# Kernel tuning notes

Hardware: AMD Instinct MI355X
Metric: run time of the kernel (lower is better)

Reference implementation:

```python
import jax, jax.numpy as jnp
import numpy as np
import math

B, S, IN_DIM = 4, 2048, 512
D, H, L, FF = 256, 4, 4, 2048
HD = D // H
EPS = 1e-5


def _pos_encoding(S, D, dtype=jnp.float32):
    pos = jnp.arange(S, dtype=jnp.float32)[:, None]
    div = jnp.exp(jnp.arange(0, D, 2, dtype=jnp.float32) * (-math.log(10000.0) / D))
    pe = jnp.zeros((S, D), dtype=jnp.float32)
    pe = pe.at[:, 0::2].set(jnp.sin(pos * div))
    pe = pe.at[:, 1::2].set(jnp.cos(pos * div))
    return pe.astype(dtype)


def _layernorm(x, w, b):
    mu = jnp.mean(x, axis=-1, keepdims=True)
    var = jnp.var(x, axis=-1, keepdims=True)
    return (x - mu) * jax.lax.rsqrt(var + EPS) * w + b


def setup_inputs() -> dict:
    key = jax.random.key(0)
    ks = jax.random.split(key, 12)
    sc = 0.02
    inp = {
        "x": jax.random.normal(ks[0], (B, S, IN_DIM), dtype=jnp.float32),
        "W_in": jax.random.normal(ks[1], (D, IN_DIM), dtype=jnp.float32) * sc,
        "b_in": jnp.zeros((D,), dtype=jnp.float32),
        "qkv_w": jax.random.normal(ks[2], (L, 3 * D, D), dtype=jnp.float32) * sc,
        "qkv_b": jnp.zeros((L, 3 * D), dtype=jnp.float32),
        "out_w": jax.random.normal(ks[3], (L, D, D), dtype=jnp.float32) * sc,
        "out_b": jnp.zeros((L, D), dtype=jnp.float32),
        "ln1_w": jnp.ones((L, D), dtype=jnp.float32),
        "ln1_b": jnp.zeros((L, D), dtype=jnp.float32),
        "ff1_w": jax.random.normal(ks[4], (L, FF, D), dtype=jnp.float32) * sc,
        "ff1_b": jnp.zeros((L, FF), dtype=jnp.float32),
        "ff2_w": jax.random.normal(ks[5], (L, D, FF), dtype=jnp.float32) * sc,
        "ff2_b": jnp.zeros((L, D), dtype=jnp.float32),
        "ln2_w": jnp.ones((L, D), dtype=jnp.float32),
        "ln2_b": jnp.zeros((L, D), dtype=jnp.float32),
        "W_fc": jax.random.normal(ks[6], (IN_DIM, D), dtype=jnp.float32) * sc,
        "b_fc": jnp.zeros((IN_DIM,), dtype=jnp.float32),
    }
    return inp


def reference(x, W_in, b_in, qkv_w, qkv_b, out_w, out_b, ln1_w, ln1_b,
              ff1_w, ff1_b, ff2_w, ff2_b, ln2_w, ln2_b, W_fc, b_fc):
    # input projection + positional encoding (dropout=0 / eval)
    h = jnp.einsum('bsi,di->bsd', x, W_in) + b_in
    h = h + _pos_encoding(S, D, h.dtype)[None]

    scale = 1.0 / math.sqrt(HD)
    for l in range(L):
        # --- self-attention (unfused: explicit QK^T + softmax + V) ---
        qkv = jnp.einsum('bsd,ed->bse', h, qkv_w[l]) + qkv_b[l]  # [B,S,3D]
        q, k, v = jnp.split(qkv, 3, axis=-1)
        q = q.reshape(B, S, H, HD).transpose(0, 2, 1, 3)  # [B,H,S,HD]
        k = k.reshape(B, S, H, HD).transpose(0, 2, 1, 3)
        v = v.reshape(B, S, H, HD).transpose(0, 2, 1, 3)
        scores = jnp.einsum('bhqd,bhkd->bhqk', q, k) * scale  # [B,H,S,S]
        attn = jax.nn.softmax(scores, axis=-1)
        ctx = jnp.einsum('bhqk,bhkd->bhqd', attn, v)
        ctx = ctx.transpose(0, 2, 1, 3).reshape(B, S, D)
        sa = jnp.einsum('bsd,ed->bse', ctx, out_w[l]) + out_b[l]
        h = _layernorm(h + sa, ln1_w[l], ln1_b[l])  # post-norm
        # --- feed-forward (relu) ---
        ff = jax.nn.relu(jnp.einsum('bsd,fd->bsf', h, ff1_w[l]) + ff1_b[l])
        ff = jnp.einsum('bsf,df->bsd', ff, ff2_w[l]) + ff2_b[l]
        h = _layernorm(h + ff, ln2_w[l], ln2_b[l])

    # final projection from last time step
    return jnp.einsum('bd,od->bo', h[:, -1, :], W_fc) + b_fc  # [B, IN_DIM]
```

## Files before the change

kernel.cpp:

```cpp
#include <hip/hip_runtime.h>
#include <math.h>

#define S_LEN 2048
#define DMODEL 256
#define NHEAD 4
#define HDIM 64
#define NLAYER 4
#define FFDIM 2048
#define INDIM 512
#define BATCH 4
#define NTOK (BATCH * S_LEN)
#define EPSV 1e-5f
#define KSPLIT 4

typedef __attribute__((ext_vector_type(8))) short frag8;
typedef __attribute__((ext_vector_type(4))) float f32x4v;
typedef unsigned short u16;
typedef unsigned int u32;

__device__ __forceinline__ float pe_val(int s, int d) {
    const float c = 0.035977892f;
    float dv = expf(-(float)(d & ~1) * c);
    float arg = (float)s * dv;
    return (d & 1) ? cosf(arg) : sinf(arg);
}

__device__ __forceinline__ u16 f2bf(float f) {
    union { float f; unsigned u; } v; v.f = f;
    unsigned r = v.u + 0x7fffu + ((v.u >> 16) & 1u);
    return (u16)(r >> 16);
}
__device__ __forceinline__ float bf2f(u16 h) {
    union { u32 u; float f; } v; v.u = (u32)h << 16; return v.f;
}
__device__ __forceinline__ u32 pk2bf(float lo, float hi) {
    union { float f; u32 u; } a, b; a.f = lo; b.f = hi;
    return __builtin_amdgcn_perm(b.u, a.u, 0x07060302u);
}
__device__ __forceinline__ void load_lds16(const u16* g, u16* l) {
    __builtin_amdgcn_global_load_lds(
        (const __attribute__((address_space(1))) unsigned int*)g,
        (__attribute__((address_space(3))) unsigned int*)l, 16, 0, 0);
}

__global__ __launch_bounds__(256) void cvt_all(
    const float* __restrict__ x, const float* __restrict__ W_in,
    const float* __restrict__ qkv_w, const float* __restrict__ out_w,
    const float* __restrict__ ff1_w, const float* __restrict__ ff2_w,
    u16* __restrict__ xb, u16* __restrict__ W_in_b,
    u16* __restrict__ qkv_w_b, u16* __restrict__ out_w_b,
    u16* __restrict__ ff1_w_b, u16* __restrict__ ff2_w_b)
{
    const int i = blockIdx.x * 256 + threadIdx.x;
    const float* src; u16* dst; int base;
    if (i < 1048576)      { src = x;     dst = xb;      base = 0; }
    else if (i < 1081344) { src = W_in;  dst = W_in_b;  base = 1048576; }
    else if (i < 1277952) { src = qkv_w; dst = qkv_w_b; base = 1081344; }
    else if (i < 1343488) { src = out_w; dst = out_w_b; base = 1277952; }
    else if (i < 1867776) { src = ff1_w; dst = ff1_w_b; base = 1343488; }
    else                  { src = ff2_w; dst = ff2_w_b; base = 1867776; }
    const int e = (i - base) * 4;
    const float4 v = *(const float4*)(src + e);
    ushort4 o;
    o.x = f2bf(v.x); o.y = f2bf(v.y); o.z = f2bf(v.z); o.w = f2bf(v.w);
    *(ushort4*)(dst + e) = o;
}

template <int MODE>
__global__ __launch_bounds__(256) void gemm_mfma(
    const u16* __restrict__ A, const u16* __restrict__ W,
    const float* __restrict__ bias, u16* __restrict__ Cb,
    int M, int N, int K)
{
    __shared__ __align__(16) u16 As[2][128 * 32];
    __shared__ __align__(16) u16 Bs[2][128 * 32];
    const int t = threadIdx.x;
    const int w = t >> 6, lane = t & 63;
    const int col = lane & 15, quad = lane >> 4;
    const int qx = (quad ^ ((col >> 1) & 3)) * 8;
    const int m0 = blockIdx.x * 128, n0 = blockIdx.y * 128;
    const int wm = (w >> 1) * 64, wn = (w & 1) * 64;

    const int r0 = lane >> 2;
    const int kc = ((lane & 3) ^ ((lane >> 3) & 3)) * 8;
    const u16* pA0 = A + (size_t)(m0 + (w * 2 + 0) * 16 + r0) * K + kc;
    const u16* pA1 = A + (size_t)(m0 + (w * 2 + 1) * 16 + r0) * K + kc;
    const u16* pB0 = W + (size_t)(n0 + (w * 2 + 0) * 16 + r0) * K + kc;
    const u16* pB1 = W + (size_t)(n0 + (w * 2 + 1) * 16 + r0) * K + kc;
    const int oA0 = (w * 2 + 0) * 512, oA1 = (w * 2 + 1) * 512;

    f32x4v acc[4][4];
#pragma unroll
    for (int i = 0; i < 4; ++i)
#pragma unroll
        for (int j = 0; j < 4; ++j) acc[i][j] = (f32x4v){0.f, 0.f, 0.f, 0.f};

    load_lds16(pA0, &As[0][oA0]);
    load_lds16(pA1, &As[0][oA1]);
    load_lds16(pB0, &Bs[0][oA0]);
    load_lds16(pB1, &Bs[0][oA1]);

    const int NIT = K >> 5;
    for (int it = 0; it < NIT; ++it) {
        const int cur = it & 1;
        __syncthreads();
        if (it + 1 < NIT) {
            const int kb = (it + 1) << 5;
            load_lds16(pA0 + kb, &As[cur ^ 1][oA0]);
            load_lds16(pA1 + kb, &As[cur ^ 1][oA1]);
            load_lds16(pB0 + kb, &Bs[cur ^ 1][oA0]);
            load_lds16(pB1 + kb, &Bs[cur ^ 1][oA1]);
        }

        frag8 a[4], b[4];
#pragma unroll
        for (int i = 0; i < 4; ++i)
            a[i] = *(const frag8*)&As[cur][(wm + i * 16 + col) * 32 + qx];
#pragma unroll
        for (int j = 0; j < 4; ++j)
            b[j] = *(const frag8*)&Bs[cur][(wn + j * 16 + col) * 32 + qx];
#pragma unroll
        for (int i = 0; i < 4; ++i)
#pragma unroll
            for (int j = 0; j < 4; ++j)
                acc[i][j] = __builtin_amdgcn_mfma_f32_16x16x32_bf16(
                    a[i], b[j], acc[i][j], 0, 0, 0);
    }

#pragma unroll
    for (int j = 0; j < 4; ++j) {
        const int cn = n0 + wn + j * 16 + col;
        const float bv = bias[cn];
#pragma unroll
        for (int i = 0; i < 4; ++i) {
            const int cmb = m0 + wm + i * 16 + quad * 4;
#pragma unroll
            for (int r = 0; r < 4; ++r) {
                float v = acc[i][j][r] + bv;
                if (MODE == 2) v = fmaxf(v, 0.f);
                Cb[(size_t)(cmb + r) * N + cn] = f2bf(v);
            }
        }
    }
}

template <int MODE>
__global__ __launch_bounds__(256) void gemm64k(
    const u16* __restrict__ A, const u16* __restrict__ W,
    const float* __restrict__ bias, u16* __restrict__ Cb,
    u16* __restrict__ aux, const float* __restrict__ lp,
    int M, int N, int K)
{
    __shared__ __align__(16) u16 As[2][64 * 64];
    __shared__ __align__(16) u16 Bs[2][64 * 64];
    const int t = threadIdx.x;
    const int w = t >> 6, lane = t & 63;
    const int col = lane & 15, quad = lane >> 4;
    const int px0 = ((quad ^ (col & 7))) * 8;
    const int px1 = px0 ^ 32;
    const int m0 = blockIdx.x * 64, n0 = blockIdx.y * 64;
    const int wm = (w >> 1) * 32, wn = (w & 1) * 32;

    const int sr = lane >> 3;
    const int lc = ((lane & 7) ^ sr) * 8;
    const u16* pA0 = A + (size_t)(m0 + w * 16 + sr) * K + lc;
    const u16* pA1 = A + (size_t)(m0 + w * 16 + 8 + sr) * K + lc;
    const u16* pB0 = W + (size_t)(n0 + w * 16 + sr) * K + lc;
    const u16* pB1 = W + (size_t)(n0 + w * 16 + 8 + sr) * K + lc;
    const int o0 = (w * 16) * 64, o1 = (w * 16 + 8) * 64;

    f32x4v acc[2][2];
#pragma unroll
    for (int i = 0; i < 2; ++i)
#pragma unroll
        for (int j = 0; j < 2; ++j) acc[i][j] = (f32x4v){0.f, 0.f, 0.f, 0.f};

    auto stageA = [&](int it, int buf) {
        if (MODE == 6) {
            const int hh = it;
#pragma unroll
            for (int pos = 0; pos < 2; ++pos) {
                const int m = m0 + w * 16 + pos * 8 + sr;
                const int q = m & (S_LEN - 1);
                const int bh = (m >> 11) * 4 + hh;
                const size_t basei = (((size_t)bh) * S_LEN + q) * 64 + lc;
                float l = 0.f;
                float o[8] = {0.f, 0.f, 0.f, 0.f, 0.f, 0.f, 0.f, 0.f};
#pragma unroll
                for (int ksx = 0; ksx < KSPLIT; ++ksx) {
                    const uint4 pv = *(const uint4*)(A + (size_t)ksx * 16 * S_LEN * 64 + basei);
                    o[0] += bf2f((u16)(pv.x & 0xffff)); o[1] += bf2f((u16)(pv.x >> 16));
                    o[2] += bf2f((u16)(pv.y & 0xffff)); o[3] += bf2f((u16)(pv.y >> 16));
                    o[4] += bf2f((u16)(pv.z & 0xffff)); o[5] += bf2f((u16)(pv.z >> 16));
                    o[6] += bf2f((u16)(pv.w & 0xffff)); o[7] += bf2f((u16)(pv.w >> 16));
                    l += lp[((size_t)ksx * 16 + bh) * S_LEN + q];
                }
                const float inv = 1.f / l;
                uint4 pk;
                pk.x = ((u32)f2bf(o[1] * inv) << 16) | f2bf(o[0] * inv);
                pk.y = ((u32)f2bf(o[3] * inv) << 16) | f2bf(o[2] * inv);
                pk.z = ((u32)f2bf(o[5] * inv) << 16) | f2bf(o[4] * inv);
                pk.w = ((u32)f2bf(o[7] * inv) << 16) | f2bf(o[6] * inv);
                *(uint4*)&As[buf][(pos ? o1 : o0) + lane * 8] = pk;
            }
        } else {
            const int kb = it << 6;
            load_lds16(pA0 + kb, &As[buf][o0]);
            load_lds16(pA1 + kb, &As[buf][o1]);
        }
    };
    auto stageB = [&](int it, int buf) {
        const int kb = it << 6;
        load_lds16(pB0 + kb, &Bs[buf][o0]);
        load_lds16(pB1 + kb, &Bs[buf][o1]);
    };

    stageA(0, 0);
    stageB(0, 0);

    const int NIT = K >> 6;
    for (int it = 0; it < NIT; ++it) {
        const int cur = it & 1;
        __syncthreads();
        if (it + 1 < NIT) {
            stageA(it + 1, cur ^ 1);
            stageB(it + 1, cur ^ 1);
        }
#pragma unroll
        for (int kh = 0; kh < 2; ++kh) {
            const int px = kh ? px1 : px0;
            frag8 a[2], b[2];
#pragma unroll
            for (int i = 0; i < 2; ++i)
                a[i] = *(const frag8*)&As[cur][(wm + i * 16 + col) * 64 + px];
#pragma unroll
            for (int j = 0; j < 2; ++j)
                b[j] = *(const frag8*)&Bs[cur][(wn + j * 16 + col) * 64 + px];
#pragma unroll
            for (int i = 0; i < 2; ++i)
#pragma unroll
                for (int j = 0; j < 2; ++j)
                    acc[i][j] = __builtin_amdgcn_mfma_f32_16x16x32_bf16(
                        a[i], b[j], acc[i][j], 0, 0, 0);
        }
    }

#pragma unroll
    for (int j = 0; j < 2; ++j) {
        const int cn = n0 + wn + j * 16 + col;
        const float bv = bias[cn];
#pragma unroll
        for (int i = 0; i < 2; ++i) {
            const int cmb = m0 + wm + i * 16 + quad * 4;
            float vv[4];
#pragma unroll
            for (int r = 0; r < 4; ++r) {
                float v = acc[i][j][r] + bv;
                if (MODE == 1) v += pe_val((cmb + r) & (S_LEN - 1), cn);
                if (MODE == 5 || MODE == 6)
                    v += bf2f(aux[(size_t)(cmb + r) * N + cn]);
                vv[r] = v;
                Cb[(size_t)(cmb + r) * N + cn] = f2bf(v);
            }
            if (MODE == 4 && cn >= 512) {
                const int dg = cn - 512;
                const int bh = (cmb >> 11) * 4 + (dg >> 6);
                uint2 pk;
                pk.x = ((u32)f2bf(vv[1]) << 16) | f2bf(vv[0]);
                pk.y = ((u32)f2bf(vv[3]) << 16) | f2bf(vv[2]);
                *(uint2*)&aux[((size_t)bh * 64 + (dg & 63)) * S_LEN + (cmb & 2047)] = pk;
            }
        }
    }
}

__global__ __launch_bounds__(256) void attn_part(const u16* __restrict__ qkv,
                                                 const u16* __restrict__ vt,
                                                 u16* __restrict__ Opart,
                                                 float* __restrict__ lpart)
{
    __shared__ __align__(16) u16 Ks[2][2][64 * 32];
    __shared__ __align__(16) u16 Vt[2][2][64 * 32];
    __shared__ __align__(16) u16 Ps[4][2][512];

    const int t = threadIdx.x;
    const int w = t >> 6, lane = t & 63;
    const int col = lane & 15, quad = lane >> 4;
    const int sq = (col >> 1) & 3;
    const int qx = (quad ^ sq) * 8;
    const int bh = blockIdx.x, b = bh >> 2, hh = bh & 3;
    const int qt = blockIdx.y, ks = blockIdx.z;

    const float SCL = 0.125f * 1.44269504f;

    frag8 qf[2][2];
#pragma unroll
    for (int qg = 0; qg < 2; ++qg) {
        const int qrow = qt * 128 + w * 32 + qg * 16 + col;
        const u16* qp = qkv + (size_t)(b * S_LEN + qrow) * 768 + hh * HDIM;
        const frag8 r0 = *(const frag8*)(qp + quad * 8);
        const frag8 r1 = *(const frag8*)(qp + 32 + quad * 8);
#pragma unroll
        for (int e = 0; e < 8; ++e) {
            qf[qg][0][e] = (short)f2bf(bf2f((u16)r0[e]) * SCL);
            qf[qg][1][e] = (short)f2bf(bf2f((u16)r1[e]) * SCL);
        }
    }
    frag8 ones;
#pragma unroll
    for (int e = 0; e < 8; ++e) ones[e] = (short)0x3F80;

    f32x4v Oacc[2][4], lacc[2];
#pragma unroll
    for (int qg = 0; qg < 2; ++qg) {
#pragma unroll
        for (int dt = 0; dt < 4; ++dt) Oacc[qg][dt] = (f32x4v){0.f, 0.f, 0.f, 0.f};
        lacc[qg] = (f32x4v){0.f, 0.f, 0.f, 0.f};
    }

    const int srow = w * 16 + (lane >> 2);
    const int sseg = ((lane & 3) ^ ((lane >> 3) & 3)) * 8;
    const int kb0 = ks * (S_LEN / KSPLIT);
    const u16* kbase = qkv + (size_t)(b * S_LEN + kb0 + srow) * 768
                       + 256 + hh * HDIM + sseg;
    const u16* vbase = vt + ((size_t)bh * 64 + srow) * S_LEN + kb0 + sseg;
    const int so = w * 512;

    load_lds16(kbase, &Ks[0][0][so]);
    load_lds16(kbase + 32, &Ks[0][1][so]);
    load_lds16(vbase, &Vt[0][0][so]);
    load_lds16(vbase + 32, &Vt[0][1][so]);

    const int NT = S_LEN / KSPLIT / 64;
    for (int kt = 0; kt < NT; ++kt) {
        const int cur = kt & 1;
        __syncthreads();
        if (kt + 1 < NT) {
            const u16* kp = kbase + (size_t)(kt + 1) * 64 * 768;
            const u16* vp = vbase + (kt + 1) * 64;
            load_lds16(kp, &Ks[cur ^ 1][0][so]);
            load_lds16(kp + 32, &Ks[cur ^ 1][1][so]);
            load_lds16(vp, &Vt[cur ^ 1][0][so]);
            load_lds16(vp + 32, &Vt[cur ^ 1][1][so]);
        }

        frag8 pf[2][2];
        uint2 held[4];
#pragma unroll
        for (int nt = 0; nt < 4; ++nt) {
            const frag8 k0 = *(const frag8*)&Ks[cur][0][(nt * 16 + col) * 32 + qx];
            const frag8 k1 = *(const frag8*)&Ks[cur][1][(nt * 16 + col) * 32 + qx];
            const int c = (nt & 1) * 2 + (quad >> 1);
            const int poff = col * 32 + ((c ^ sq) * 8) + (quad & 1) * 4;

            f32x4v s0 = (f32x4v){0.f, 0.f, 0.f, 0.f};
            s0 = __builtin_amdgcn_mfma_f32_16x16x32_bf16(k0, qf[0][0], s0, 0, 0, 0);
            s0 = __builtin_amdgcn_mfma_f32_16x16x32_bf16(k1, qf[0][1], s0, 0, 0, 0);
            f32x4v s1 = (f32x4v){0.f, 0.f, 0.f, 0.f};
            s1 = __builtin_amdgcn_mfma_f32_16x16x32_bf16(k0, qf[1][0], s1, 0, 0, 0);
            s1 = __builtin_amdgcn_mfma_f32_16x16x32_bf16(k1, qf[1][1], s1, 0, 0, 0);

            uint2 pk;
            pk.x = pk2bf(__builtin_amdgcn_exp2f(s0[0]), __builtin_amdgcn_exp2f(s0[1]));
            pk.y = pk2bf(__builtin_amdgcn_exp2f(s0[2]), __builtin_amdgcn_exp2f(s0[3]));
            *(uint2*)&Ps[w][nt >> 1][poff] = pk;

            held[nt].x = pk2bf(__builtin_amdgcn_exp2f(s1[0]), __builtin_amdgcn_exp2f(s1[1]));
            held[nt].y = pk2bf(__builtin_amdgcn_exp2f(s1[2]), __builtin_amdgcn_exp2f(s1[3]));
        }
        pf[0][0] = *(const frag8*)&Ps[w][0][col * 32 + qx];
        pf[0][1] = *(const frag8*)&Ps[w][1][col * 32 + qx];
#pragma unroll
        for (int nt = 0; nt < 4; ++nt) {
            const int c = (nt & 1) * 2 + (quad >> 1);
            const int poff = col * 32 + ((c ^ sq) * 8) + (quad & 1) * 4;
            *(uint2*)&Ps[w][nt >> 1][poff] = held[nt];
        }
        pf[1][0] = *(const frag8*)&Ps[w][0][col * 32 + qx];
        pf[1][1] = *(const frag8*)&Ps[w][1][col * 32 + qx];

#pragma unroll
        for (int dt = 0; dt < 4; ++dt) {
            const frag8 v0 = *(const frag8*)&Vt[cur][0][(dt * 16 + col) * 32 + qx];
            const frag8 v1 = *(const frag8*)&Vt[cur][1][(dt * 16 + col) * 32 + qx];
#pragma unroll
            for (int qg = 0; qg < 2; ++qg) {
                Oacc[qg][dt] = __builtin_amdgcn_mfma_f32_16x16x32_bf16(
                    v0, pf[qg][0], Oacc[qg][dt], 0, 0, 0);
                Oacc[qg][dt] = __builtin_amdgcn_mfma_f32_16x16x32_bf16(
                    v1, pf[qg][1], Oacc[qg][dt], 0, 0, 0);
            }
        }
#pragma unroll
        for (int qg = 0; qg < 2; ++qg) {
            lacc[qg] = __builtin_amdgcn_mfma_f32_16x16x32_bf16(
                ones, pf[qg][0], lacc[qg], 0, 0, 0);
            lacc[qg] = __builtin_amdgcn_mfma_f32_16x16x32_bf16(
                ones, pf[qg][1], lacc[qg], 0, 0, 0);
        }
    }

#pragma unroll
    for (int qg = 0; qg < 2; ++qg) {
        const int qrow = qt * 128 + w * 32 + qg * 16 + col;
        u16* op = Opart + (((size_t)ks * 16 + bh) * S_LEN + qrow) * 64;
#pragma unroll
        for (int dt = 0; dt < 4; ++dt) {
            uint2 pk;
            pk.x = pk2bf(Oacc[qg][dt][0], Oacc[qg][dt][1]);
            pk.y = pk2bf(Oacc[qg][dt][2], Oacc[qg][dt][3]);
            *(uint2*)(op + dt * 16 + quad * 4) = pk;
        }
        if (quad == 0)
            lpart[((size_t)ks * 16 + bh) * S_LEN + qrow] = lacc[qg][0];
    }
}

__global__ __launch_bounds__(256) void ln_wave(u16* __restrict__ hb,
                                               const u16* __restrict__ sab,
                                               const float* __restrict__ w,
                                               const float* __restrict__ b)
{
    const int t = threadIdx.x;
    const int wv = t >> 6, lane = t & 63;
    const int row = blockIdx.x * 4 + wv;
    const size_t base = (size_t)row * DMODEL + lane * 4;

    const ushort4 xv = *(const ushort4*)&sab[base];
    const float x0 = bf2f(xv.x), x1 = bf2f(xv.y);
    const float x2 = bf2f(xv.z), x3 = bf2f(xv.w);

    float s = (x0 + x1) + (x2 + x3);
    float s2 = (x0 * x0 + x1 * x1) + (x2 * x2 + x3 * x3);
#pragma unroll
    for (int msk = 1; msk < 64; msk <<= 1) {
        s += __shfl_xor(s, msk);
        s2 += __shfl_xor(s2, msk);
    }
    const float mu = s * (1.f / DMODEL);
    const float var = s2 * (1.f / DMODEL) - mu * mu;
    const float rs = rsqrtf(var + EPSV);

    const float4 wv4 = *(const float4*)&w[lane * 4];
    const float4 bv4 = *(const float4*)&b[lane * 4];
    ushort4 o;
    o.x = f2bf((x0 - mu) * rs * wv4.x + bv4.x);
    o.y = f2bf((x1 - mu) * rs * wv4.y + bv4.y);
    o.z = f2bf((x2 - mu) * rs * wv4.z + bv4.z);
    o.w = f2bf((x3 - mu) * rs * wv4.w + bv4.w);
    *(ushort4*)&hb[base] = o;
}

__global__ __launch_bounds__(256) void final_proj(const u16* __restrict__ hb,
                                                  const float* __restrict__ Wfc,
                                                  const float* __restrict__ bfc,
                                                  float* __restrict__ out)
{
    const int idx = blockIdx.x * 256 + threadIdx.x;
    const int b = idx >> 9;
    const int o = idx & 511;
    const u16* hp = hb + (size_t)(b * S_LEN + S_LEN - 1) * DMODEL;
    const float* wp = Wfc + (size_t)o * DMODEL;
    float s = 0.f;
#pragma unroll 4
    for (int d = 0; d < DMODEL; ++d) s += bf2f(hp[d]) * wp[d];
    out[idx] = s + bfc[o];
}

extern "C" void kernel_launch(void* const* d_in, const int* in_sizes, int n_in,
                              void* d_out, int out_size, void* d_ws, size_t ws_size,
                              hipStream_t stream)
{
    const float* x     = (const float*)d_in[0];
    const float* W_in  = (const float*)d_in[1];
    const float* b_in  = (const float*)d_in[2];
    const float* qkv_w = (const float*)d_in[3];
    const float* qkv_b = (const float*)d_in[4];
    const float* out_w = (const float*)d_in[5];
    const float* out_b = (const float*)d_in[6];
    const float* ln1_w = (const float*)d_in[7];
    const float* ln1_b = (const float*)d_in[8];
    const float* ff1_w = (const float*)d_in[9];
    const float* ff1_b = (const float*)d_in[10];
    const float* ff2_w = (const float*)d_in[11];
    const float* ff2_b = (const float*)d_in[12];
    const float* ln2_w = (const float*)d_in[13];
    const float* ln2_b = (const float*)d_in[14];
    const float* W_fc  = (const float*)d_in[15];
    const float* b_fc  = (const float*)d_in[16];
    float* out = (float*)d_out;

    char* p = (char*)d_ws;
    u16* hb    = (u16*)p;  p += (size_t)NTOK * DMODEL * 2;
    u16* sab   = (u16*)p;  p += (size_t)NTOK * DMODEL * 2;
    u16* xb    = (u16*)p;  p += (size_t)NTOK * INDIM * 2;
    u16* qkvb  = (u16*)p;  p += (size_t)NTOK * 768 * 2;
    u16* ffb   = (u16*)p;  p += (size_t)NTOK * FFDIM * 2;
    u16* vtb   = (u16*)p;  p += (size_t)16 * 64 * S_LEN * 2;
    float* lpart = (float*)p; p += (size_t)KSPLIT * 16 * S_LEN * 4;
    u16* W_in_b  = (u16*)p; p += (size_t)131072 * 2;
    u16* qkv_w_b = (u16*)p; p += (size_t)786432 * 2;
    u16* out_w_b = (u16*)p; p += (size_t)262144 * 2;
    u16* ff1_w_b = (u16*)p; p += (size_t)2097152 * 2;
    u16* ff2_w_b = (u16*)p; p += (size_t)2097152 * 2;
    if (ws_size < (size_t)78643200) return;

    u16* Opart = ffb;

    cvt_all<<<9344, 256, 0, stream>>>(x, W_in, qkv_w, out_w, ff1_w, ff2_w,
                                      xb, W_in_b, qkv_w_b, out_w_b, ff1_w_b, ff2_w_b);

    gemm64k<1><<<dim3(NTOK / 64, DMODEL / 64), 256, 0, stream>>>(
        xb, W_in_b, b_in, hb, nullptr, nullptr, NTOK, DMODEL, INDIM);

    for (int l = 0; l < NLAYER; ++l) {
        gemm64k<4><<<dim3(NTOK / 64, 768 / 64), 256, 0, stream>>>(
            hb, qkv_w_b + (size_t)l * 768 * DMODEL, qkv_b + l * 768,
            qkvb, vtb, nullptr, NTOK, 768, DMODEL);
        attn_part<<<dim3(BATCH * NHEAD, S_LEN / 128, KSPLIT), 256, 0, stream>>>(
            qkvb, vtb, Opart, lpart);
        gemm64k<6><<<dim3(NTOK / 64, DMODEL / 64), 256, 0, stream>>>(
            Opart, out_w_b + (size_t)l * DMODEL * DMODEL, out_b + l * DMODEL,
            sab, hb, lpart, NTOK, DMODEL, DMODEL);
        ln_wave<<<NTOK / 4, 256, 0, stream>>>(hb, sab, ln1_w + l * DMODEL, ln1_b + l * DMODEL);
        gemm_mfma<2><<<dim3(NTOK / 128, FFDIM / 128), 256, 0, stream>>>(
            hb, ff1_w_b + (size_t)l * FFDIM * DMODEL, ff1_b + l * FFDIM,
            ffb, NTOK, FFDIM, DMODEL);
        gemm64k<5><<<dim3(NTOK / 64, DMODEL / 64), 256, 0, stream>>>(
            ffb, ff2_w_b + (size_t)l * DMODEL * FFDIM, ff2_b + l * DMODEL,
            sab, hb, nullptr, NTOK, DMODEL, FFDIM);
        ln_wave<<<NTOK / 4, 256, 0, stream>>>(hb, sab, ln2_w + l * DMODEL, ln2_b + l * DMODEL);
    }

    final_proj<<<8, 256, 0, stream>>>(hb, W_fc, b_fc, out);
}
```

Baseline: 525.3 us.

## Keep attention probabilities in registers via 16x16x16 MFMA, drop LDS round-trip

Replaces the LDS staging of the softmax probability tile with direct register reuse. The S accumulator layout already matches the B-operand layout of the 16x16x16 bf16 MFMA, so P is fed to PV as 4-element fragments and V is read from LDS with a matching swizzled offset. The row-sum is now accumulated in fp32 from the exp values with cross-lane shuffles, replacing the ones-matrix MFMA. The cost is twice as many smaller MFMA instructions for PV. The row-sum now uses unrounded fp32 values instead of the bf16-rounded probabilities.

```diff
diff --git a/kernel.cpp b/kernel.cpp
--- a/kernel.cpp
+++ b/kernel.cpp
@@ -14,6 +14,7 @@
 #define KSPLIT 4
 
 typedef __attribute__((ext_vector_type(8))) short frag8;
+typedef __attribute__((ext_vector_type(4))) short frag4;
 typedef __attribute__((ext_vector_type(4))) float f32x4v;
 typedef unsigned short u16;
 typedef unsigned int u32;
@@ -281,7 +282,6 @@
 {
     __shared__ __align__(16) u16 Ks[2][2][64 * 32];
     __shared__ __align__(16) u16 Vt[2][2][64 * 32];
-    __shared__ __align__(16) u16 Ps[4][2][512];
 
     const int t = threadIdx.x;
     const int w = t >> 6, lane = t & 63;
@@ -306,17 +306,13 @@
             qf[qg][1][e] = (short)f2bf(bf2f((u16)r1[e]) * SCL);
         }
     }
-    frag8 ones;
-#pragma unroll
-    for (int e = 0; e < 8; ++e) ones[e] = (short)0x3F80;
-
-    f32x4v Oacc[2][4], lacc[2];
-#pragma unroll
-    for (int qg = 0; qg < 2; ++qg) {
+
+    f32x4v Oacc[2][4];
+    float psum[2] = {0.f, 0.f};
+#pragma unroll
+    for (int qg = 0; qg < 2; ++qg)
 #pragma unroll
         for (int dt = 0; dt < 4; ++dt) Oacc[qg][dt] = (f32x4v){0.f, 0.f, 0.f, 0.f};
-        lacc[qg] = (f32x4v){0.f, 0.f, 0.f, 0.f};
-    }
 
     const int srow = w * 16 + (lane >> 2);
     const int sseg = ((lane & 3) ^ ((lane >> 3) & 3)) * 8;
@@ -344,14 +340,11 @@
             load_lds16(vp + 32, &Vt[cur ^ 1][1][so]);
         }
 
-        frag8 pf[2][2];
-        uint2 held[4];
+        frag4 pfr[2][4];
 #pragma unroll
         for (int nt = 0; nt < 4; ++nt) {
             const frag8 k0 = *(const frag8*)&Ks[cur][0][(nt * 16 + col) * 32 + qx];
             const frag8 k1 = *(const frag8*)&Ks[cur][1][(nt * 16 + col) * 32 + qx];
-            const int c = (nt & 1) * 2 + (quad >> 1);
-            const int poff = col * 32 + ((c ^ sq) * 8) + (quad & 1) * 4;
 
             f32x4v s0 = (f32x4v){0.f, 0.f, 0.f, 0.f};
             s0 = __builtin_amdgcn_mfma_f32_16x16x32_bf16(k0, qf[0][0], s0, 0, 0, 0);
@@ -360,48 +353,48 @@
             s1 = __builtin_amdgcn_mfma_f32_16x16x32_bf16(k0, qf[1][0], s1, 0, 0, 0);
             s1 = __builtin_amdgcn_mfma_f32_16x16x32_bf16(k1, qf[1][1], s1, 0, 0, 0);
 
-            uint2 pk;
-            pk.x = pk2bf(__builtin_amdgcn_exp2f(s0[0]), __builtin_amdgcn_exp2f(s0[1]));
-            pk.y = pk2bf(__builtin_amdgcn_exp2f(s0[2]), __builtin_amdgcn_exp2f(s0[3]));
-            *(uint2*)&Ps[w][nt >> 1][poff] = pk;
-
-            held[nt].x = pk2bf(__builtin_amdgcn_exp2f(s1[0]), __builtin_amdgcn_exp2f(s1[1]));
-            held[nt].y = pk2bf(__builtin_amdgcn_exp2f(s1[2]), __builtin_amdgcn_exp2f(s1[3]));
-        }
-        pf[0][0] = *(const frag8*)&Ps[w][0][col * 32 + qx];
-        pf[0][1] = *(const frag8*)&Ps[w][1][col * 32 + qx];
-#pragma unroll
-        for (int nt = 0; nt < 4; ++nt) {
-            const int c = (nt & 1) * 2 + (quad >> 1);
-            const int poff = col * 32 + ((c ^ sq) * 8) + (quad & 1) * 4;
-            *(uint2*)&Ps[w][nt >> 1][poff] = held[nt];
-        }
-        pf[1][0] = *(const frag8*)&Ps[w][0][col * 32 + qx];
-        pf[1][1] = *(const frag8*)&Ps[w][1][col * 32 + qx];
+            const float a0 = __builtin_amdgcn_exp2f(s0[0]);
+            const float a1 = __builtin_amdgcn_exp2f(s0[1]);
+            const float a2 = __builtin_amdgcn_exp2f(s0[2]);
+            const float a3 = __builtin_amdgcn_exp2f(s0[3]);
+            psum[0] += (a0 + a1) + (a2 + a3);
+            union { uint2 u; frag4 f; } c0;
+            c0.u.x = pk2bf(a0, a1);
+            c0.u.y = pk2bf(a2, a3);
+            pfr[0][nt] = c0.f;
+
+            const float b0 = __builtin_amdgcn_exp2f(s1[0]);
+            const float b1 = __builtin_amdgcn_exp2f(s1[1]);
+            const float b2 = __builtin_amdgcn_exp2f(s1[2]);
+            const float b3 = __builtin_amdgcn_exp2f(s1[3]);
+            psum[1] += (b0 + b1) + (b2 + b3);
+            union { uint2 u; frag4 f; } c1;
+            c1.u.x = pk2bf(b0, b1);
+            c1.u.y = pk2bf(b2, b3);
+            pfr[1][nt] = c1.f;
+        }
 
 #pragma unroll
         for (int dt = 0; dt < 4; ++dt) {
-            const frag8 v0 = *(const frag8*)&Vt[cur][0][(dt * 16 + col) * 32 + qx];
-            const frag8 v1 = *(const frag8*)&Vt[cur][1][(dt * 16 + col) * 32 + qx];
-#pragma unroll
-            for (int qg = 0; qg < 2; ++qg) {
-                Oacc[qg][dt] = __builtin_amdgcn_mfma_f32_16x16x32_bf16(
-                    v0, pf[qg][0], Oacc[qg][dt], 0, 0, 0);
-                Oacc[qg][dt] = __builtin_amdgcn_mfma_f32_16x16x32_bf16(
-                    v1, pf[qg][1], Oacc[qg][dt], 0, 0, 0);
+#pragma unroll
+            for (int kg = 0; kg < 4; ++kg) {
+                const int voff = (dt * 16 + col) * 32
+                               + ((((kg & 1) * 2 + (quad >> 1)) ^ sq) << 3)
+                               + ((quad & 1) << 2);
+                const frag4 vf = *(const frag4*)&Vt[cur][kg >> 1][voff];
+                Oacc[0][dt] = __builtin_amdgcn_mfma_f32_16x16x16bf16_1k(
+                    vf, pfr[0][kg], Oacc[0][dt], 0, 0, 0);
+                Oacc[1][dt] = __builtin_amdgcn_mfma_f32_16x16x16bf16_1k(
+                    vf, pfr[1][kg], Oacc[1][dt], 0, 0, 0);
             }
         }
-#pragma unroll
-        for (int qg = 0; qg < 2; ++qg) {
-            lacc[qg] = __builtin_amdgcn_mfma_f32_16x16x32_bf16(
-                ones, pf[qg][0], lacc[qg], 0, 0, 0);
-            lacc[qg] = __builtin_amdgcn_mfma_f32_16x16x32_bf16(
-                ones, pf[qg][1], lacc[qg], 0, 0, 0);
-        }
     }
 
 #pragma unroll
     for (int qg = 0; qg < 2; ++qg) {
+        float ls = psum[qg];
+        ls += __shfl_xor(ls, 16);
+        ls += __shfl_xor(ls, 32);
         const int qrow = qt * 128 + w * 32 + qg * 16 + col;
         u16* op = Opart + (((size_t)ks * 16 + bh) * S_LEN + qrow) * 64;
 #pragma unroll
@@ -412,7 +405,7 @@
             *(uint2*)(op + dt * 16 + quad * 4) = pk;
         }
         if (quad == 0)
-            lpart[((size_t)ks * 16 + bh) * S_LEN + qrow] = lacc[qg][0];
+            lpart[((size_t)ks * 16 + bh) * S_LEN + qrow] = ls;
     }
 }
 
```

After: 530.7 us. No clear change (+1.0%).
